# Optimization experiments

Hardware: AMD Instinct MI355X
Metric: run time of the kernel (lower is better)

The kernel has to match this reference:

```python
import jax, jax.numpy as jnp
from jax import lax
import numpy as np

B, T, D, H, L = 512, 1024, 5, 128, 16


def _u(key, shape, fan):
    bound = 1.0 / np.sqrt(fan)
    return jax.random.uniform(key, shape, jnp.float32, -bound, bound)


def setup_inputs() -> dict:
    key = jax.random.key(0)
    ks = jax.random.split(key, 16)
    return {
        "x": jax.random.normal(ks[0], (B, T, D), jnp.float32),
        # encoder GRU (PyTorch layout: rows ordered [reset; update; new])
        "enc_W_ih": _u(ks[1], (3 * H, D), H),
        "enc_W_hh": _u(ks[2], (3 * H, H), H),
        "enc_b_ih": _u(ks[3], (3 * H,), H),
        "enc_b_hh": _u(ks[4], (3 * H,), H),
        # encoder_fc: hidden -> latent
        "enc_fc_W": _u(ks[5], (L, H), H),
        "enc_fc_b": _u(ks[6], (L,), H),
        # decoder_fc: latent -> hidden
        "dec_fc_W": _u(ks[7], (H, L), L),
        "dec_fc_b": _u(ks[8], (H,), L),
        # decoder GRU (input size = hidden_dim)
        "dec_W_ih": _u(ks[9], (3 * H, H), H),
        "dec_W_hh": _u(ks[10], (3 * H, H), H),
        "dec_b_ih": _u(ks[11], (3 * H,), H),
        "dec_b_hh": _u(ks[12], (3 * H,), H),
        # output_fc: hidden -> input_dim
        "out_W": _u(ks[13], (D, H), H),
        "out_b": _u(ks[14], (D,), H),
    }


def _gru_step(W_hh, b_hh, h, xp):
    # xp: precomputed input projection [B, 3H]; PyTorch GRU cell math
    hp = h @ W_hh.T + b_hh
    r = jax.nn.sigmoid(xp[:, :H] + hp[:, :H])
    zg = jax.nn.sigmoid(xp[:, H:2 * H] + hp[:, H:2 * H])
    n = jnp.tanh(xp[:, 2 * H:] + r * hp[:, 2 * H:])
    return (1.0 - zg) * n + zg * h


def reference(x, enc_W_ih, enc_W_hh, enc_b_ih, enc_b_hh, enc_fc_W, enc_fc_b,
              dec_fc_W, dec_fc_b, dec_W_ih, dec_W_hh, dec_b_ih, dec_b_hh,
              out_W, out_b):
    b, t, _ = x.shape
    # ---- encode: precompute all input projections, scan the recurrence ----
    xp_enc = jnp.einsum('btd,gd->tbg', x, enc_W_ih) + enc_b_ih  # [T,B,3H]
    h0 = jnp.zeros((b, H), x.dtype)
    h_n, _ = lax.scan(lambda h, xp: (_gru_step(enc_W_hh, enc_b_hh, h, xp), None),
                      h0, xp_enc)
    z = h_n @ enc_fc_W.T + enc_fc_b  # [B,L]
    # ---- decode: constant repeated input => one shared input projection ----
    h_dec_in = z @ dec_fc_W.T + dec_fc_b  # [B,H]
    xp_dec = h_dec_in @ dec_W_ih.T + dec_b_ih  # [B,3H], same every step

    def dec_step(h, _):
        h_new = _gru_step(dec_W_hh, dec_b_hh, h, xp_dec)
        return h_new, h_new

    _, hs = lax.scan(dec_step, jnp.zeros((b, H), x.dtype), None, length=t)  # [T,B,H]
    recon = jnp.einsum('tbh,dh->btd', hs, out_W) + out_b  # [B,T,D]
    return recon, z
```

## Files before the change

kernel.cpp:

```cpp
#include <hip/hip_runtime.h>

#define Hd 128
#define Tn 1024
#define Dn 5
#define Ln 16
#define Bn 512
#define QP 36
#define HP4 144
#define GF(f) ((f) + (((f) >> 5) << 2))
#define CF(q) (QP * ((q) >> 3) + 4 * ((q) & 7))

__device__ __forceinline__ float sigm(float x) { return 1.0f / (1.0f + __expf(-x)); }
__device__ __forceinline__ float tanh_fast(float x) { return 1.0f - 2.0f / (1.0f + __expf(2.0f * x)); }

#define RED4(v) { v += __shfl_xor(v, 1); v += __shfl_xor(v, 2); }

__global__ __launch_bounds__(512)
__attribute__((amdgpu_waves_per_eu(2, 2)))
void gru_ae_kernel(
    const float* __restrict__ x,
    const float* __restrict__ eWih, const float* __restrict__ eWhh,
    const float* __restrict__ ebih, const float* __restrict__ ebhh,
    const float* __restrict__ efcW, const float* __restrict__ efcb,
    const float* __restrict__ dfcW, const float* __restrict__ dfcb,
    const float* __restrict__ dWih, const float* __restrict__ dWhh,
    const float* __restrict__ dbih, const float* __restrict__ dbhh,
    const float* __restrict__ oW, const float* __restrict__ ob,
    float* __restrict__ out)
{
    __shared__ __align__(16) float henc[2][HP4];
    __shared__ __align__(16) float hs[32][HP4];
    __shared__ __align__(16) float hdi[HP4];
    __shared__ float zl[Ln];

    const int tid = threadIdx.x;
    const int j   = tid >> 2;
    const int kq  = tid & 3;
    const int b   = blockIdx.x;
    const int koff = kq * 32;
    const int klds = kq * QP;

    float4 wr[8], wz[8], wn[8];
    {
        const float4* p0 = (const float4*)(eWhh + (size_t)j * Hd + koff);
        const float4* p1 = (const float4*)(eWhh + (size_t)(Hd + j) * Hd + koff);
        const float4* p2 = (const float4*)(eWhh + (size_t)(2 * Hd + j) * Hd + koff);
#pragma unroll
        for (int k = 0; k < 8; ++k) { wr[k] = p0[k]; wz[k] = p1[k]; wn[k] = p2[k]; }
    }
    const int d0s = (kq == 1) ? 2 : (kq == 2) ? 4 : 0;
    const int inc = (kq < 2) ? 1 : 0;
    const float m0 = (kq < 3) ? 1.f : 0.f, m1 = (kq < 2) ? 1.f : 0.f;
    float wxr0 = m0 * eWih[(size_t)j * Dn + d0s];
    float wxr1 = m1 * eWih[(size_t)j * Dn + d0s + inc];
    float wxz0 = m0 * eWih[(size_t)(Hd + j) * Dn + d0s];
    float wxz1 = m1 * eWih[(size_t)(Hd + j) * Dn + d0s + inc];
    float wxn0 = m0 * eWih[(size_t)(2 * Hd + j) * Dn + d0s];
    float wxn1 = m1 * eWih[(size_t)(2 * Hd + j) * Dn + d0s + inc];

    float bR = ebih[j] + ebhh[j];
    float bZ = ebih[Hd + j] + ebhh[Hd + j];
    float bihn = ebih[2 * Hd + j];
    float bhhn = ebhh[2 * Hd + j];

    if (tid < Hd) { henc[0][GF(tid)] = 0.f; henc[1][GF(tid)] = 0.f; }
    __syncthreads();

    float h_self = 0.f;
    int p = 0;
    const float* xrow = x + (size_t)b * Tn * Dn;
    float xc0 = xrow[d0s], xc1 = xrow[d0s + inc];

#pragma unroll 1
    for (int t = 0; t < Tn; ++t) {
        const int off = ((t + 1 < Tn) ? (t + 1) : (Tn - 1)) * Dn;
        float nx0 = xrow[off + d0s], nx1 = xrow[off + d0s + inc];

        const float4* hv = (const float4*)&henc[p][klds];
        float ar = 0.f, az = 0.f, nh = 0.f;
#pragma unroll
        for (int k = 0; k < 8; ++k) {
            float4 h4 = hv[k];
            ar = fmaf(wr[k].x, h4.x, ar); az = fmaf(wz[k].x, h4.x, az); nh = fmaf(wn[k].x, h4.x, nh);
            ar = fmaf(wr[k].y, h4.y, ar); az = fmaf(wz[k].y, h4.y, az); nh = fmaf(wn[k].y, h4.y, nh);
            ar = fmaf(wr[k].z, h4.z, ar); az = fmaf(wz[k].z, h4.z, az); nh = fmaf(wn[k].z, h4.z, nh);
            ar = fmaf(wr[k].w, h4.w, ar); az = fmaf(wz[k].w, h4.w, az); nh = fmaf(wn[k].w, h4.w, nh);
        }
        ar = fmaf(wxr0, xc0, fmaf(wxr1, xc1, ar));
        az = fmaf(wxz0, xc0, fmaf(wxz1, xc1, az));
        float nx = fmaf(wxn0, xc0, wxn1 * xc1);
        RED4(ar); RED4(az); RED4(nh); RED4(nx);
        float r  = sigm(ar + bR);
        float zg = sigm(az + bZ);
        float n  = tanh_fast(nx + bihn + r * (nh + bhhn));
        float hnew = fmaf(zg, h_self - n, n);
        h_self = hnew;
        if (!kq) henc[p ^ 1][GF(j)] = hnew;
        xc0 = nx0; xc1 = nx1;
        __syncthreads();
        p ^= 1;
    }

    if (tid < Ln) {
        const float4* wp = (const float4*)(efcW + (size_t)tid * Hd);
        float acc = efcb[tid];
#pragma unroll
        for (int q = 0; q < 32; ++q) {
            float4 w4 = wp[q];
            float4 h4 = *(const float4*)&henc[p][CF(q)];
            acc = fmaf(w4.x, h4.x, fmaf(w4.y, h4.y, fmaf(w4.z, h4.z, fmaf(w4.w, h4.w, acc))));
        }
        out[(size_t)Bn * Tn * Dn + (size_t)b * Ln + tid] = acc;
        zl[tid] = acc;
    }
    __syncthreads();

    if (tid < Hd) {
        const float4* wp = (const float4*)(dfcW + (size_t)tid * Ln);
        float acc = dfcb[tid];
#pragma unroll
        for (int l = 0; l < 4; ++l) {
            float4 w4 = wp[l];
            acc = fmaf(w4.x, zl[4 * l + 0], acc);
            acc = fmaf(w4.y, zl[4 * l + 1], acc);
            acc = fmaf(w4.z, zl[4 * l + 2], acc);
            acc = fmaf(w4.w, zl[4 * l + 3], acc);
        }
        hdi[GF(tid)] = acc;
    }
    __syncthreads();

    float xdr, xdz, xdn;
    {
        const float4* p0 = (const float4*)(dWih + (size_t)j * Hd + koff);
        const float4* p1 = (const float4*)(dWih + (size_t)(Hd + j) * Hd + koff);
        const float4* p2 = (const float4*)(dWih + (size_t)(2 * Hd + j) * Hd + koff);
#pragma unroll
        for (int k = 0; k < 8; ++k) { wr[k] = p0[k]; wz[k] = p1[k]; wn[k] = p2[k]; }
        const float4* hv = (const float4*)&hdi[klds];
        float a0 = 0.f, a1 = 0.f, a2 = 0.f;
#pragma unroll
        for (int k = 0; k < 8; ++k) {
            float4 h4 = hv[k];
            a0 = fmaf(wr[k].x, h4.x, a0); a1 = fmaf(wz[k].x, h4.x, a1); a2 = fmaf(wn[k].x, h4.x, a2);
            a0 = fmaf(wr[k].y, h4.y, a0); a1 = fmaf(wz[k].y, h4.y, a1); a2 = fmaf(wn[k].y, h4.y, a2);
            a0 = fmaf(wr[k].z, h4.z, a0); a1 = fmaf(wz[k].z, h4.z, a1); a2 = fmaf(wn[k].z, h4.z, a2);
            a0 = fmaf(wr[k].w, h4.w, a0); a1 = fmaf(wz[k].w, h4.w, a1); a2 = fmaf(wn[k].w, h4.w, a2);
        }
        RED4(a0); RED4(a1); RED4(a2);
        xdr = a0 + dbih[j] + dbhh[j];
        xdz = a1 + dbih[Hd + j] + dbhh[Hd + j];
        xdn = a2 + dbih[2 * Hd + j];
        bhhn = dbhh[2 * Hd + j];
    }

    {
        const float4* p0 = (const float4*)(dWhh + (size_t)j * Hd + koff);
        const float4* p1 = (const float4*)(dWhh + (size_t)(Hd + j) * Hd + koff);
        const float4* p2 = (const float4*)(dWhh + (size_t)(2 * Hd + j) * Hd + koff);
#pragma unroll
        for (int k = 0; k < 8; ++k) { wr[k] = p0[k]; wz[k] = p1[k]; wn[k] = p2[k]; }
    }

    if (tid < Hd) hs[31][GF(tid)] = 0.f;
    h_self = 0.f;
    __syncthreads();

#pragma unroll 1
    for (int s0 = 0; s0 < Tn; s0 += 32) {
#pragma unroll 1
        for (int ss = 0; ss < 32; ++ss) {
            const int ip = (ss + 31) & 31;
            const float4* hv = (const float4*)&hs[ip][klds];
            float ar = 0.f, az = 0.f, nh = 0.f;
#pragma unroll
            for (int k = 0; k < 8; ++k) {
                float4 h4 = hv[k];
                ar = fmaf(wr[k].x, h4.x, ar); az = fmaf(wz[k].x, h4.x, az); nh = fmaf(wn[k].x, h4.x, nh);
                ar = fmaf(wr[k].y, h4.y, ar); az = fmaf(wz[k].y, h4.y, az); nh = fmaf(wn[k].y, h4.y, nh);
                ar = fmaf(wr[k].z, h4.z, ar); az = fmaf(wz[k].z, h4.z, az); nh = fmaf(wn[k].z, h4.z, nh);
                ar = fmaf(wr[k].w, h4.w, ar); az = fmaf(wz[k].w, h4.w, az); nh = fmaf(wn[k].w, h4.w, nh);
            }
            RED4(ar); RED4(az); RED4(nh);
            float r  = sigm(xdr + ar);
            float zg = sigm(xdz + az);
            float n  = tanh_fast(xdn + r * (nh + bhhn));
            float hnew = fmaf(zg, h_self - n, n);
            h_self = hnew;
            if (!kq) hs[ss][GF(j)] = hnew;
            __syncthreads();
        }

        if (tid < 160) {
            const int i = tid / 5, d = tid % 5;
            const float4* wrow = (const float4*)(oW + (size_t)d * Hd);
            float ac0 = ob[d], ac1 = 0.f;
#pragma unroll
            for (int q = 0; q < 32; q += 2) {
                const int qa = (q + i) & 31, qb = (q + 1 + i) & 31;
                float4 ha = *(const float4*)&hs[i][CF(qa)];
                float4 wa = wrow[qa];
                float4 hb = *(const float4*)&hs[i][CF(qb)];
                float4 wb = wrow[qb];
                ac0 = fmaf(wa.x, ha.x, fmaf(wa.y, ha.y, fmaf(wa.z, ha.z, fmaf(wa.w, ha.w, ac0))));
                ac1 = fmaf(wb.x, hb.x, fmaf(wb.y, hb.y, fmaf(wb.z, hb.z, fmaf(wb.w, hb.w, ac1))));
            }
            out[((size_t)b * Tn + s0 + i) * Dn + d] = ac0 + ac1;
        }
        __syncthreads();
    }
}

extern "C" void kernel_launch(void* const* d_in, const int* in_sizes, int n_in,
                              void* d_out, int out_size, void* d_ws, size_t ws_size,
                              hipStream_t stream) {
    const float* x    = (const float*)d_in[0];
    const float* eWih = (const float*)d_in[1];
    const float* eWhh = (const float*)d_in[2];
    const float* ebih = (const float*)d_in[3];
    const float* ebhh = (const float*)d_in[4];
    const float* efcW = (const float*)d_in[5];
    const float* efcb = (const float*)d_in[6];
    const float* dfcW = (const float*)d_in[7];
    const float* dfcb = (const float*)d_in[8];
    const float* dWih = (const float*)d_in[9];
    const float* dWhh = (const float*)d_in[10];
    const float* dbih = (const float*)d_in[11];
    const float* dbhh = (const float*)d_in[12];
    const float* oW   = (const float*)d_in[13];
    const float* ob   = (const float*)d_in[14];
    float* out = (float*)d_out;

    gru_ae_kernel<<<dim3(Bn), dim3(512), 0, stream>>>(
        x, eWih, eWhh, ebih, ebhh, efcW, efcb, dfcW, dfcb,
        dWih, dWhh, dbih, dbhh, oW, ob, out);
}
```

Measured before the change: 2.991 ms.

## Process two batch rows per block to reuse register-resident GRU weights

Each block now runs the encoder and decoder recurrences for two batch rows at once, reusing the same register-held W_hh slices for both dot products, and the grid is halved to 256 blocks. This halves the weight loads and per-step barriers per sequence and gives each step two independent dependency chains to interleave, which hides latency. In exchange, per-step work per block doubles, shared memory use doubles, and only 256 blocks exist, which may underfill the 256 CUs on MI355X. Register pressure also grows.

```diff
diff --git a/kernel.cpp b/kernel.cpp
--- a/kernel.cpp
+++ b/kernel.cpp
@@ -14,6 +14,16 @@
 __device__ __forceinline__ float tanh_fast(float x) { return 1.0f - 2.0f / (1.0f + __expf(2.0f * x)); }
 
 #define RED4(v) { v += __shfl_xor(v, 1); v += __shfl_xor(v, 2); }
+
+#define QDOT(hv, AR, AZ, NH)                                                     \
+    _Pragma("unroll")                                                            \
+    for (int k = 0; k < 8; ++k) {                                                \
+        float4 h4 = (hv)[k];                                                     \
+        AR = fmaf(wr[k].x, h4.x, AR); AZ = fmaf(wz[k].x, h4.x, AZ); NH = fmaf(wn[k].x, h4.x, NH); \
+        AR = fmaf(wr[k].y, h4.y, AR); AZ = fmaf(wz[k].y, h4.y, AZ); NH = fmaf(wn[k].y, h4.y, NH); \
+        AR = fmaf(wr[k].z, h4.z, AR); AZ = fmaf(wz[k].z, h4.z, AZ); NH = fmaf(wn[k].z, h4.z, NH); \
+        AR = fmaf(wr[k].w, h4.w, AR); AZ = fmaf(wz[k].w, h4.w, AZ); NH = fmaf(wn[k].w, h4.w, NH); \
+    }
 
 __global__ __launch_bounds__(512)
 __attribute__((amdgpu_waves_per_eu(2, 2)))
@@ -28,15 +38,15 @@
     const float* __restrict__ oW, const float* __restrict__ ob,
     float* __restrict__ out)
 {
-    __shared__ __align__(16) float henc[2][HP4];
-    __shared__ __align__(16) float hs[32][HP4];
-    __shared__ __align__(16) float hdi[HP4];
-    __shared__ float zl[Ln];
+    __shared__ __align__(16) float henc[2][2][HP4];
+    __shared__ __align__(16) float hs[2][32][HP4];
+    __shared__ __align__(16) float hdi[2][HP4];
+    __shared__ float zl[2][Ln];
 
     const int tid = threadIdx.x;
     const int j   = tid >> 2;
     const int kq  = tid & 3;
-    const int b   = blockIdx.x;
+    const int b0  = blockIdx.x * 2;
     const int koff = kq * 32;
     const int klds = kq * QP;
 
@@ -63,94 +73,100 @@
     float bihn = ebih[2 * Hd + j];
     float bhhn = ebhh[2 * Hd + j];
 
-    if (tid < Hd) { henc[0][GF(tid)] = 0.f; henc[1][GF(tid)] = 0.f; }
-    __syncthreads();
-
-    float h_self = 0.f;
+    if (tid < 2 * Hd) {
+        const int rp = tid >> 7, f = tid & 127;
+        henc[0][rp][GF(f)] = 0.f; henc[1][rp][GF(f)] = 0.f;
+    }
+    __syncthreads();
+
+    float h0 = 0.f, h1 = 0.f;
     int p = 0;
-    const float* xrow = x + (size_t)b * Tn * Dn;
-    float xc0 = xrow[d0s], xc1 = xrow[d0s + inc];
+    const float* xt0 = x + (size_t)b0 * Tn * Dn;
+    const float* xt1 = xt0 + (size_t)Tn * Dn;
 
 #pragma unroll 1
     for (int t = 0; t < Tn; ++t) {
-        const int off = ((t + 1 < Tn) ? (t + 1) : (Tn - 1)) * Dn;
-        float nx0 = xrow[off + d0s], nx1 = xrow[off + d0s + inc];
-
-        const float4* hv = (const float4*)&henc[p][klds];
-        float ar = 0.f, az = 0.f, nh = 0.f;
-#pragma unroll
-        for (int k = 0; k < 8; ++k) {
-            float4 h4 = hv[k];
-            ar = fmaf(wr[k].x, h4.x, ar); az = fmaf(wz[k].x, h4.x, az); nh = fmaf(wn[k].x, h4.x, nh);
-            ar = fmaf(wr[k].y, h4.y, ar); az = fmaf(wz[k].y, h4.y, az); nh = fmaf(wn[k].y, h4.y, nh);
-            ar = fmaf(wr[k].z, h4.z, ar); az = fmaf(wz[k].z, h4.z, az); nh = fmaf(wn[k].z, h4.z, nh);
-            ar = fmaf(wr[k].w, h4.w, ar); az = fmaf(wz[k].w, h4.w, az); nh = fmaf(wn[k].w, h4.w, nh);
-        }
-        ar = fmaf(wxr0, xc0, fmaf(wxr1, xc1, ar));
-        az = fmaf(wxz0, xc0, fmaf(wxz1, xc1, az));
-        float nx = fmaf(wxn0, xc0, wxn1 * xc1);
-        RED4(ar); RED4(az); RED4(nh); RED4(nx);
-        float r  = sigm(ar + bR);
-        float zg = sigm(az + bZ);
-        float n  = tanh_fast(nx + bihn + r * (nh + bhhn));
-        float hnew = fmaf(zg, h_self - n, n);
-        h_self = hnew;
-        if (!kq) henc[p ^ 1][GF(j)] = hnew;
-        xc0 = nx0; xc1 = nx1;
+        float xa0 = xt0[d0s], xa1 = xt0[d0s + inc];
+        float xb0 = xt1[d0s], xb1 = xt1[d0s + inc];
+        xt0 += Dn; xt1 += Dn;
+
+        const float4* hv0 = (const float4*)&henc[p][0][klds];
+        const float4* hv1 = (const float4*)&henc[p][1][klds];
+        float ar0 = 0.f, az0 = 0.f, nh0 = 0.f;
+        float ar1 = 0.f, az1 = 0.f, nh1 = 0.f;
+        QDOT(hv0, ar0, az0, nh0)
+        QDOT(hv1, ar1, az1, nh1)
+
+        ar0 = fmaf(wxr0, xa0, fmaf(wxr1, xa1, ar0));
+        az0 = fmaf(wxz0, xa0, fmaf(wxz1, xa1, az0));
+        float nx0 = fmaf(wxn0, xa0, wxn1 * xa1);
+        ar1 = fmaf(wxr0, xb0, fmaf(wxr1, xb1, ar1));
+        az1 = fmaf(wxz0, xb0, fmaf(wxz1, xb1, az1));
+        float nx1 = fmaf(wxn0, xb0, wxn1 * xb1);
+        RED4(ar0); RED4(az0); RED4(nh0); RED4(nx0);
+        RED4(ar1); RED4(az1); RED4(nh1); RED4(nx1);
+
+        float r0 = sigm(ar0 + bR), z0 = sigm(az0 + bZ);
+        float n0 = tanh_fast(nx0 + bihn + r0 * (nh0 + bhhn));
+        float hn0 = fmaf(z0, h0 - n0, n0);
+        float r1 = sigm(ar1 + bR), z1 = sigm(az1 + bZ);
+        float n1 = tanh_fast(nx1 + bihn + r1 * (nh1 + bhhn));
+        float hn1 = fmaf(z1, h1 - n1, n1);
+        h0 = hn0; h1 = hn1;
+        if (!kq) { henc[p ^ 1][0][GF(j)] = hn0; henc[p ^ 1][1][GF(j)] = hn1; }
         __syncthreads();
         p ^= 1;
     }
 
-    if (tid < Ln) {
-        const float4* wp = (const float4*)(efcW + (size_t)tid * Hd);
-        float acc = efcb[tid];
+    if (tid < 2 * Ln) {
+        const int rp = tid >> 4, l = tid & 15;
+        const float4* wp = (const float4*)(efcW + (size_t)l * Hd);
+        float acc = efcb[l];
 #pragma unroll
         for (int q = 0; q < 32; ++q) {
             float4 w4 = wp[q];
-            float4 h4 = *(const float4*)&henc[p][CF(q)];
+            float4 h4 = *(const float4*)&henc[p][rp][CF(q)];
             acc = fmaf(w4.x, h4.x, fmaf(w4.y, h4.y, fmaf(w4.z, h4.z, fmaf(w4.w, h4.w, acc))));
         }
-        out[(size_t)Bn * Tn * Dn + (size_t)b * Ln + tid] = acc;
-        zl[tid] = acc;
-    }
-    __syncthreads();
-
-    if (tid < Hd) {
-        const float4* wp = (const float4*)(dfcW + (size_t)tid * Ln);
-        float acc = dfcb[tid];
+        out[(size_t)Bn * Tn * Dn + (size_t)(b0 + rp) * Ln + l] = acc;
+        zl[rp][l] = acc;
+    }
+    __syncthreads();
+
+    if (tid < 2 * Hd) {
+        const int rp = tid >> 7, f = tid & 127;
+        const float4* wp = (const float4*)(dfcW + (size_t)f * Ln);
+        float acc = dfcb[f];
 #pragma unroll
         for (int l = 0; l < 4; ++l) {
             float4 w4 = wp[l];
-            acc = fmaf(w4.x, zl[4 * l + 0], acc);
-            acc = fmaf(w4.y, zl[4 * l + 1], acc);
-            acc = fmaf(w4.z, zl[4 * l + 2], acc);
-            acc = fmaf(w4.w, zl[4 * l + 3], acc);
-        }
-        hdi[GF(tid)] = acc;
-    }
-    __syncthreads();
-
-    float xdr, xdz, xdn;
+            acc = fmaf(w4.x, zl[rp][4 * l + 0], acc);
+            acc = fmaf(w4.y, zl[rp][4 * l + 1], acc);
+            acc = fmaf(w4.z, zl[rp][4 * l + 2], acc);
+            acc = fmaf(w4.w, zl[rp][4 * l + 3], acc);
+        }
+        hdi[rp][GF(f)] = acc;
+    }
+    __syncthreads();
+
+    float xdr0, xdz0, xdn0, xdr1, xdz1, xdn1;
     {
         const float4* p0 = (const float4*)(dWih + (size_t)j * Hd + koff);
         const float4* p1 = (const float4*)(dWih + (size_t)(Hd + j) * Hd + koff);
         const float4* p2 = (const float4*)(dWih + (size_t)(2 * Hd + j) * Hd + koff);
 #pragma unroll
         for (int k = 0; k < 8; ++k) { wr[k] = p0[k]; wz[k] = p1[k]; wn[k] = p2[k]; }
-        const float4* hv = (const float4*)&hdi[klds];
-        float a0 = 0.f, a1 = 0.f, a2 = 0.f;
-#pragma unroll
-        for (int k = 0; k < 8; ++k) {
-            float4 h4 = hv[k];
-            a0 = fmaf(wr[k].x, h4.x, a0); a1 = fmaf(wz[k].x, h4.x, a1); a2 = fmaf(wn[k].x, h4.x, a2);
-            a0 = fmaf(wr[k].y, h4.y, a0); a1 = fmaf(wz[k].y, h4.y, a1); a2 = fmaf(wn[k].y, h4.y, a2);
-            a0 = fmaf(wr[k].z, h4.z, a0); a1 = fmaf(wz[k].z, h4.z, a1); a2 = fmaf(wn[k].z, h4.z, a2);
-            a0 = fmaf(wr[k].w, h4.w, a0); a1 = fmaf(wz[k].w, h4.w, a1); a2 = fmaf(wn[k].w, h4.w, a2);
-        }
-        RED4(a0); RED4(a1); RED4(a2);
-        xdr = a0 + dbih[j] + dbhh[j];
-        xdz = a1 + dbih[Hd + j] + dbhh[Hd + j];
-        xdn = a2 + dbih[2 * Hd + j];
+        const float4* hv0 = (const float4*)&hdi[0][klds];
+        const float4* hv1 = (const float4*)&hdi[1][klds];
+        float a0 = 0.f, a1 = 0.f, a2 = 0.f, c0 = 0.f, c1 = 0.f, c2 = 0.f;
+        QDOT(hv0, a0, a1, a2)
+        QDOT(hv1, c0, c1, c2)
+        RED4(a0); RED4(a1); RED4(a2); RED4(c0); RED4(c1); RED4(c2);
+        const float br_ = dbih[j] + dbhh[j];
+        const float bz_ = dbih[Hd + j] + dbhh[Hd + j];
+        const float bn_ = dbih[2 * Hd + j];
+        xdr0 = a0 + br_; xdz0 = a1 + bz_; xdn0 = a2 + bn_;
+        xdr1 = c0 + br_; xdz1 = c1 + bz_; xdn1 = c2 + bn_;
         bhhn = dbhh[2 * Hd + j];
     }
 
@@ -162,8 +178,11 @@
         for (int k = 0; k < 8; ++k) { wr[k] = p0[k]; wz[k] = p1[k]; wn[k] = p2[k]; }
     }
 
-    if (tid < Hd) hs[31][GF(tid)] = 0.f;
-    h_self = 0.f;
+    if (tid < 2 * Hd) {
+        const int rp = tid >> 7, f = tid & 127;
+        hs[rp][31][GF(f)] = 0.f;
+    }
+    h0 = 0.f; h1 = 0.f;
     __syncthreads();
 
 #pragma unroll 1
@@ -171,41 +190,41 @@
 #pragma unroll 1
         for (int ss = 0; ss < 32; ++ss) {
             const int ip = (ss + 31) & 31;
-            const float4* hv = (const float4*)&hs[ip][klds];
-            float ar = 0.f, az = 0.f, nh = 0.f;
-#pragma unroll
-            for (int k = 0; k < 8; ++k) {
-                float4 h4 = hv[k];
-                ar = fmaf(wr[k].x, h4.x, ar); az = fmaf(wz[k].x, h4.x, az); nh = fmaf(wn[k].x, h4.x, nh);
-                ar = fmaf(wr[k].y, h4.y, ar); az = fmaf(wz[k].y, h4.y, az); nh = fmaf(wn[k].y, h4.y, nh);
-                ar = fmaf(wr[k].z, h4.z, ar); az = fmaf(wz[k].z, h4.z, az); nh = fmaf(wn[k].z, h4.z, nh);
-                ar = fmaf(wr[k].w, h4.w, ar); az = fmaf(wz[k].w, h4.w, az); nh = fmaf(wn[k].w, h4.w, nh);
-            }
-            RED4(ar); RED4(az); RED4(nh);
-            float r  = sigm(xdr + ar);
-            float zg = sigm(xdz + az);
-            float n  = tanh_fast(xdn + r * (nh + bhhn));
-            float hnew = fmaf(zg, h_self - n, n);
-            h_self = hnew;
-            if (!kq) hs[ss][GF(j)] = hnew;
+            const float4* hv0 = (const float4*)&hs[0][ip][klds];
+            const float4* hv1 = (const float4*)&hs[1][ip][klds];
+            float ar0 = 0.f, az0 = 0.f, nh0 = 0.f;
+            float ar1 = 0.f, az1 = 0.f, nh1 = 0.f;
+            QDOT(hv0, ar0, az0, nh0)
+            QDOT(hv1, ar1, az1, nh1)
+            RED4(ar0); RED4(az0); RED4(nh0);
+            RED4(ar1); RED4(az1); RED4(nh1);
+            float r0 = sigm(xdr0 + ar0), z0 = sigm(xdz0 + az0);
+            float n0 = tanh_fast(xdn0 + r0 * (nh0 + bhhn));
+            float hn0 = fmaf(z0, h0 - n0, n0);
+            float r1 = sigm(xdr1 + ar1), z1 = sigm(xdz1 + az1);
+            float n1 = tanh_fast(xdn1 + r1 * (nh1 + bhhn));
+            float hn1 = fmaf(z1, h1 - n1, n1);
+            h0 = hn0; h1 = hn1;
+            if (!kq) { hs[0][ss][GF(j)] = hn0; hs[1][ss][GF(j)] = hn1; }
             __syncthreads();
         }
 
-        if (tid < 160) {
-            const int i = tid / 5, d = tid % 5;
+        if (tid < 320) {
+            const int rowp = tid / 160, o = tid % 160;
+            const int i = o / 5, d = o % 5;
             const float4* wrow = (const float4*)(oW + (size_t)d * Hd);
             float ac0 = ob[d], ac1 = 0.f;
 #pragma unroll
             for (int q = 0; q < 32; q += 2) {
                 const int qa = (q + i) & 31, qb = (q + 1 + i) & 31;
-                float4 ha = *(const float4*)&hs[i][CF(qa)];
+                float4 ha = *(const float4*)&hs[rowp][i][CF(qa)];
                 float4 wa = wrow[qa];
-                float4 hb = *(const float4*)&hs[i][CF(qb)];
+                float4 hb = *(const float4*)&hs[rowp][i][CF(qb)];
                 float4 wb = wrow[qb];
                 ac0 = fmaf(wa.x, ha.x, fmaf(wa.y, ha.y, fmaf(wa.z, ha.z, fmaf(wa.w, ha.w, ac0))));
                 ac1 = fmaf(wb.x, hb.x, fmaf(wb.y, hb.y, fmaf(wb.z, hb.z, fmaf(wb.w, hb.w, ac1))));
             }
-            out[((size_t)b * Tn + s0 + i) * Dn + d] = ac0 + ac1;
+            out[((size_t)(b0 + rowp) * Tn + s0 + i) * Dn + d] = ac0 + ac1;
         }
         __syncthreads();
     }
@@ -231,7 +250,7 @@
     const float* ob   = (const float*)d_in[14];
     float* out = (float*)d_out;
 
-    gru_ae_kernel<<<dim3(Bn), dim3(512), 0, stream>>>(
+    gru_ae_kernel<<<dim3(Bn / 2), dim3(512), 0, stream>>>(
         x, eWih, eWhh, ebih, ebhh, efcW, efcb, dfcW, dfcb,
         dWih, dWhh, dbih, dbhh, oW, ob, out);
 }
```

Result: no change. 2.947 ms (-1.5%).
